# Kernel optimization log

Hardware: AMD Instinct MI355X
Metric: run time of the kernel (lower is better)

The kernel has to match this reference:

```python
import jax, jax.numpy as jnp
import numpy as np

N, M, D_IN, D_OUT = 100000, 1024, 64, 64


def setup_inputs() -> dict:
    key = jax.random.key(0)
    ks = jax.random.split(key, 8)
    # kaiming_uniform_ bound for fan_in = D_IN: sqrt(6 / fan_in) with a=sqrt(5) default? torch's
    # kaiming_uniform_ default (a=0) gives bound = sqrt(6/fan_in); exact init is irrelevant for math.
    bound = float(np.sqrt(6.0 / D_IN))
    return {
        "x": jax.random.normal(ks[0], (N, D_IN), dtype=jnp.float32),
        "neighbors": jax.random.normal(ks[1], (M, D_IN), dtype=jnp.float32),
        "Wq": jax.random.uniform(ks[2], (D_OUT, D_IN), jnp.float32, -bound, bound),
        "bq": jnp.zeros((D_OUT,), jnp.float32),
        "Wk": jax.random.uniform(ks[3], (D_OUT, D_IN), jnp.float32, -bound, bound),
        "bk": jnp.zeros((D_OUT,), jnp.float32),
        "Wv": jax.random.uniform(ks[4], (D_OUT, D_IN), jnp.float32, -bound, bound),
        "bv": jnp.zeros((D_OUT,), jnp.float32),
    }


def reference(x, neighbors, Wq, bq, Wk, bk, Wv, bv):
    # q: [N, D_OUT], k: [M, D_OUT]
    q = x @ Wq.T + bq
    k = neighbors @ Wk.T + bk
    # scores: [N, M] -- same math as sum(q[:,None,:] * k[None,:,:], axis=2) but via GEMM
    scores = q @ k.T
    attn = jax.nn.softmax(scores, axis=1)
    # attn @ neighbors: [N, D_IN], then value projection -> [N, D_OUT]
    agg = attn @ neighbors
    return agg @ Wv.T + bv
```

## Files before the change

### kernel.cpp

```cpp
#include <hip/hip_runtime.h>


#define N_ROWS 100000
#define VT_STRIDE 1040

typedef __attribute__((ext_vector_type(8))) _Float16 half8;
typedef __attribute__((ext_vector_type(4))) float    f32x4;

#define MFMA16(a,b,c) __builtin_amdgcn_mfma_f32_16x16x32_f16((a),(b),(c),0,0,0)

static __device__ __forceinline__ f32x4 zero4() {
    f32x4 v = {0.f, 0.f, 0.f, 0.f};
    return v;
}

__global__ __launch_bounds__(256)
void prep_kernel(const float* __restrict__ nb, const float* __restrict__ Wq,
                 const float* __restrict__ bq, const float* __restrict__ Wk,
                 unsigned short* __restrict__ Gh, unsigned short* __restrict__ Gl,
                 float* __restrict__ uW, unsigned short* __restrict__ Kp,
                 unsigned short* __restrict__ VTp)
{
    __shared__ __align__(16) float sm[8192];
    const int tid = threadIdx.x;
    if (blockIdx.x == 0) {
        const float4* wk4 = (const float4*)Wk;
        const float4* wq4 = (const float4*)Wq;
        float4* dk = (float4*)sm;
        float4* dq = (float4*)(sm + 4096);
        #pragma unroll
        for (int u = 0; u < 4; u++) {
            dk[u * 256 + tid] = wk4[u * 256 + tid];
            dq[u * 256 + tid] = wq4[u * 256 + tid];
        }
        __syncthreads();
        const int e2 = tid & 63, e1g = (tid >> 6) * 16;
        float g[16];
        #pragma unroll
        for (int q = 0; q < 16; q++) g[q] = 0.f;
        for (int w = 0; w < 64; w++) {
            float kv = sm[w * 64 + e2];
            const float* wqp = sm + 4096 + w * 64 + e1g;
            #pragma unroll
            for (int q = 0; q < 16; q++) g[q] = fmaf(wqp[q], kv, g[q]);
        }
        union { half8 h; uint4 u; } ph0, pl0, ph1, pl1;
        #pragma unroll
        for (int i = 0; i < 8; i++) {
            _Float16 h0 = (_Float16)g[i];
            ph0.h[i] = h0; pl0.h[i] = (_Float16)(g[i] - (float)h0);
            _Float16 h1 = (_Float16)g[8 + i];
            ph1.h[i] = h1; pl1.h[i] = (_Float16)(g[8 + i] - (float)h1);
        }
        *(uint4*)(Gh + e2 * 72 + e1g)     = ph0.u;
        *(uint4*)(Gh + e2 * 72 + e1g + 8) = ph1.u;
        *(uint4*)(Gl + e2 * 72 + e1g)     = pl0.u;
        *(uint4*)(Gl + e2 * 72 + e1g + 8) = pl1.u;
        if (tid < 64) {
            float uu = 0.f;
            for (int w = 0; w < 64; w++) uu = fmaf(bq[w], sm[w * 64 + tid], uu);
            uW[tid] = uu;
        }
    } else {
        const int j0 = (blockIdx.x - 1) * 64;
        const int jr = tid >> 2;
        const int c0 = (tid & 3) * 16;
        const float* np = nb + (size_t)(j0 + jr) * 64 + c0;
        float a[16];
        #pragma unroll
        for (int u = 0; u < 4; u++) *(float4*)(a + 4 * u) = *(const float4*)(np + 4 * u);
        const int pr = (jr & ~31) | (((jr >> 2) & 1) << 4) | (((jr >> 3) & 3) << 2) | (jr & 3);
        union { half8 h; uint4 u; } pk0, pk1;
        #pragma unroll
        for (int i = 0; i < 8; i++) { pk0.h[i] = (_Float16)a[i]; pk1.h[i] = (_Float16)a[8 + i]; }
        *(uint4*)(Kp + (size_t)(j0 + pr) * 72 + c0)     = pk0.u;
        *(uint4*)(Kp + (size_t)(j0 + pr) * 72 + c0 + 8) = pk1.u;
        #pragma unroll
        for (int i = 0; i < 16; i++) sm[jr * 65 + c0 + i] = a[i];
        __syncthreads();
        const int d   = tid >> 2;
        const int jc0 = (tid & 3) * 16;
        union { half8 h; uint4 u; } pv0, pv1;
        #pragma unroll
        for (int i = 0; i < 8; i++) {
            pv0.h[i] = (_Float16)sm[(jc0 + i) * 65 + d];
            pv1.h[i] = (_Float16)sm[(jc0 + 8 + i) * 65 + d];
        }
        *(uint4*)(VTp + (size_t)d * VT_STRIDE + j0 + jc0)     = pv0.u;
        *(uint4*)(VTp + (size_t)d * VT_STRIDE + j0 + jc0 + 8) = pv1.u;
    }
}

__global__ __launch_bounds__(256, 3)
void attn_kernel(const float* __restrict__ x,
                 const unsigned short* __restrict__ Gh,
                 const unsigned short* __restrict__ Gl,
                 const float* __restrict__ uW,
                 const unsigned short* __restrict__ Kp,
                 const unsigned short* __restrict__ VTp,
                 const float* __restrict__ Wv,
                 const float* __restrict__ bv,
                 float* __restrict__ out)
{
    __shared__ __align__(16) float slices[4 * 1088];
    const int tid  = threadIdx.x;
    const int lane = tid & 63;
    const int wv   = tid >> 6;
    const int Q    = lane >> 4;
    const int c    = lane & 15;
    const int rbase = blockIdx.x * 128 + wv * 32;
    float* slice = slices + wv * 1088;

    half8 qh[2][2], ql[2][2];
    #pragma unroll
    for (int rt = 0; rt < 2; rt++) {
        int row = rbase + rt * 16 + c;
        if (row > N_ROWS - 1) row = N_ROWS - 1;
        half8 xh[2], xl[2];
        #pragma unroll
        for (int ks = 0; ks < 2; ks++) {
            const float* xp = x + (size_t)row * 64 + ks * 32 + Q * 8;
            float a[8];
            *(float4*)a       = *(const float4*)xp;
            *(float4*)(a + 4) = *(const float4*)(xp + 4);
            #pragma unroll
            for (int i = 0; i < 8; i++) {
                _Float16 h = (_Float16)a[i];
                xh[ks][i] = h;
                xl[ks][i] = (_Float16)(a[i] - (float)h);
            }
        }
        #pragma unroll
        for (int mt = 0; mt < 4; mt++) {
            f32x4 Cm = zero4();
            #pragma unroll
            for (int ks = 0; ks < 2; ks++) {
                half8 gh = *(const half8*)(Gh + (mt * 16 + c) * 72 + ks * 32 + Q * 8);
                half8 gl = *(const half8*)(Gl + (mt * 16 + c) * 72 + ks * 32 + Q * 8);
                Cm = MFMA16(gh, xh[ks], Cm);
                Cm = MFMA16(gh, xl[ks], Cm);
                Cm = MFMA16(gl, xh[ks], Cm);
            }
            *(f32x4*)(slice + c * 68 + mt * 16 + 4 * Q) = Cm;
        }
        __builtin_amdgcn_s_waitcnt(0);
        #pragma unroll
        for (int ks = 0; ks < 2; ks++) {
            const float* qp = slice + c * 68 + ks * 32 + Q * 8;
            const float* up = uW + ks * 32 + Q * 8;
            #pragma unroll
            for (int i = 0; i < 8; i++) {
                float val = qp[i] + up[i];
                _Float16 h = (_Float16)val;
                qh[rt][ks][i] = h;
                ql[rt][ks][i] = (_Float16)(val - (float)h);
            }
        }
        __builtin_amdgcn_s_waitcnt(0);
    }

    f32x4 acc[2][4];
    #pragma unroll
    for (int qt = 0; qt < 2; qt++)
        #pragma unroll
        for (int dt = 0; dt < 4; dt++) acc[qt][dt] = zero4();
    float mrow[2] = { -3.0e38f, -3.0e38f };
    float lrow[2] = { 0.f, 0.f };

    #pragma unroll 2
    for (int jc = 0; jc < 32; jc++) {
        const int jb = jc * 32;
        half8 k0[2], k1[2];
        #pragma unroll
        for (int t = 0; t < 2; t++) {
            const unsigned short* kp = Kp + (size_t)(jb + 16 * t + c) * 72;
            k0[t] = *(const half8*)(kp + Q * 8);
            k1[t] = *(const half8*)(kp + 32 + Q * 8);
        }
        half8 vA[4];
        #pragma unroll
        for (int dt = 0; dt < 4; dt++)
            vA[dt] = *(const half8*)(VTp + (size_t)(dt * 16 + c) * VT_STRIDE + jb + Q * 8);

        f32x4 S[2][2];
        #pragma unroll
        for (int t = 0; t < 2; t++) {
            #pragma unroll
            for (int qt = 0; qt < 2; qt++) {
                f32x4 s = MFMA16(k0[t], qh[qt][0], zero4());
                s = MFMA16(k1[t], qh[qt][1], s);
                s = MFMA16(k0[t], ql[qt][0], s);
                s = MFMA16(k1[t], ql[qt][1], s);
                S[t][qt] = s;
            }
        }
        half8 pB[2];
        #pragma unroll
        for (int qt = 0; qt < 2; qt++) {
            float cm = fmaxf(fmaxf(fmaxf(S[0][qt][0], S[0][qt][1]),
                                   fmaxf(S[0][qt][2], S[0][qt][3])),
                             fmaxf(fmaxf(S[1][qt][0], S[1][qt][1]),
                                   fmaxf(S[1][qt][2], S[1][qt][3])));
            cm = fmaxf(cm, __shfl_xor(cm, 16));
            cm = fmaxf(cm, __shfl_xor(cm, 32));
            if (__any(cm > mrow[qt] + 8.f)) {
                const float mn = fmaxf(mrow[qt], cm);
                const float sc = __expf(mrow[qt] - mn);
                mrow[qt] = mn;
                lrow[qt] *= sc;
                #pragma unroll
                for (int dt = 0; dt < 4; dt++)
                    #pragma unroll
                    for (int r = 0; r < 4; r++) acc[qt][dt][r] *= sc;
            }
            const float mref = mrow[qt];
            float p[8]; float ps = 0.f;
            #pragma unroll
            for (int r = 0; r < 4; r++) { p[r] = __expf(S[0][qt][r] - mref); ps += p[r]; }
            #pragma unroll
            for (int r = 0; r < 4; r++) { p[4 + r] = __expf(S[1][qt][r] - mref); ps += p[4 + r]; }
            ps += __shfl_xor(ps, 16);
            ps += __shfl_xor(ps, 32);
            lrow[qt] += ps;
            #pragma unroll
            for (int i = 0; i < 8; i++) pB[qt][i] = (_Float16)p[i];
        }
        #pragma unroll
        for (int dt = 0; dt < 4; dt++) {
            acc[0][dt] = MFMA16(vA[dt], pB[0], acc[0][dt]);
            acc[1][dt] = MFMA16(vA[dt], pB[1], acc[1][dt]);
        }
    }

    #pragma unroll
    for (int qt = 0; qt < 2; qt++) {
        const float rl = 1.f / lrow[qt];
        #pragma unroll
        for (int dt = 0; dt < 4; dt++)
            #pragma unroll
            for (int r = 0; r < 4; r++) acc[qt][dt][r] *= rl;
    }
    half8 wf[4][2];
    #pragma unroll
    for (int mt = 0; mt < 4; mt++)
        #pragma unroll
        for (int ks = 0; ks < 2; ks++) {
            const float* wp = Wv + (size_t)(mt * 16 + c) * 64 + ks * 32 + Q * 8;
            #pragma unroll
            for (int i = 0; i < 8; i++) wf[mt][ks][i] = (_Float16)wp[i];
        }
    const int srcA = 32 * (Q & 1) + c;
    const int srcB = srcA + 16;
    const bool hi = (Q >> 1) & 1;
    f32x4 o[2][4];
    #pragma unroll
    for (int qt = 0; qt < 2; qt++) {
        half8 pe[2];
        #pragma unroll
        for (int ks = 0; ks < 2; ks++) {
            #pragma unroll
            for (int r = 0; r < 4; r++) {
                float a0 = __shfl(acc[qt][2 * ks + 0][r], srcA);
                float a1 = __shfl(acc[qt][2 * ks + 1][r], srcA);
                float b0 = __shfl(acc[qt][2 * ks + 0][r], srcB);
                float b1 = __shfl(acc[qt][2 * ks + 1][r], srcB);
                pe[ks][r]     = (_Float16)(hi ? a1 : a0);
                pe[ks][4 + r] = (_Float16)(hi ? b1 : b0);
            }
        }
        #pragma unroll
        for (int mt = 0; mt < 4; mt++) {
            f32x4 t = MFMA16(wf[mt][0], pe[0], zero4());
            o[qt][mt] = MFMA16(wf[mt][1], pe[1], t);
        }
    }
    float4 bf[4];
    #pragma unroll
    for (int mt = 0; mt < 4; mt++) bf[mt] = *(const float4*)(bv + mt * 16 + 4 * Q);
    #pragma unroll
    for (int qt = 0; qt < 2; qt++) {
        const int row = rbase + qt * 16 + c;
        if (row < N_ROWS) {
            #pragma unroll
            for (int mt = 0; mt < 4; mt++) {
                float4 vv = make_float4(o[qt][mt][0] + bf[mt].x, o[qt][mt][1] + bf[mt].y,
                                        o[qt][mt][2] + bf[mt].z, o[qt][mt][3] + bf[mt].w);
                *(float4*)(out + (size_t)row * 64 + mt * 16 + 4 * Q) = vv;
            }
        }
    }
}

extern "C" void kernel_launch(void* const* d_in, const int* in_sizes, int n_in,
                              void* d_out, int out_size, void* d_ws, size_t ws_size,
                              hipStream_t stream)
{
    const float* x  = (const float*)d_in[0];
    const float* nb = (const float*)d_in[1];
    const float* Wq = (const float*)d_in[2];
    const float* bq = (const float*)d_in[3];
    const float* Wk = (const float*)d_in[4];
    const float* Wv = (const float*)d_in[6];
    const float* bv = (const float*)d_in[7];
    float* out = (float*)d_out;

    char* ws = (char*)d_ws;
    unsigned short* Gh  = (unsigned short*)(ws);
    unsigned short* Gl  = (unsigned short*)(ws + 9216);
    float*          uW  = (float*)(ws + 18432);
    unsigned short* Kp  = (unsigned short*)(ws + 18688);
    unsigned short* VTp = (unsigned short*)(ws + 166144);

    prep_kernel<<<17, 256, 0, stream>>>(nb, Wq, bq, Wk, Gh, Gl, uW, Kp, VTp);
    const int grid = (N_ROWS + 127) / 128;
    attn_kernel<<<grid, 256, 0, stream>>>(x, Gh, Gl, uW, Kp, VTp, Wv, bv, out);
}
```

Baseline: 167.4 us.

## Use single-wave blocks, double-buffer K fragments, and defer row-sum reduction

Reshapes the attention kernel from 256-thread blocks covering 128 rows to 64-thread single-wave blocks covering 32 rows. The main loop becomes a manually double-buffered flash step that prefetches the next K tile while computing on the current one. The row-sum shuffle reduction moves out of the loop to the end, and the max shuffle now runs only when a rescale is needed. The goals are to hide K load latency and cut cross-lane shuffles per iteration, at the cost of more blocks, more register pressure from the prefetch buffers, and a grid that assumes N is divisible by 32.

```diff
diff --git a/kernel.cpp b/kernel.cpp
--- a/kernel.cpp
+++ b/kernel.cpp
@@ -91,7 +91,73 @@
     }
 }
 
-__global__ __launch_bounds__(256, 3)
+static __device__ __forceinline__ void flash_step(
+    int jb, int jn, int c, int Q,
+    const unsigned short* __restrict__ Kp, const unsigned short* __restrict__ VTp,
+    const half8 (&ck0)[2], const half8 (&ck1)[2],
+    half8 (&nk0)[2], half8 (&nk1)[2],
+    const half8 (&qh)[2][2], const half8 (&ql)[2][2],
+    f32x4 (&acc)[2][4], float (&mrow)[2], float (&lrow)[2])
+{
+    half8 vA[4];
+    #pragma unroll
+    for (int dt = 0; dt < 4; dt++)
+        vA[dt] = *(const half8*)(VTp + (size_t)(dt * 16 + c) * VT_STRIDE + jb + Q * 8);
+    #pragma unroll
+    for (int t = 0; t < 2; t++) {
+        const unsigned short* kp = Kp + (size_t)(jn + 16 * t + c) * 72;
+        nk0[t] = *(const half8*)(kp + Q * 8);
+        nk1[t] = *(const half8*)(kp + 32 + Q * 8);
+    }
+    f32x4 S[2][2];
+    #pragma unroll
+    for (int t = 0; t < 2; t++)
+        #pragma unroll
+        for (int qt = 0; qt < 2; qt++) {
+            f32x4 s = MFMA16(ck0[t], qh[qt][0], zero4());
+            s = MFMA16(ck1[t], qh[qt][1], s);
+            s = MFMA16(ck0[t], ql[qt][0], s);
+            s = MFMA16(ck1[t], ql[qt][1], s);
+            S[t][qt] = s;
+        }
+    half8 pB[2];
+    #pragma unroll
+    for (int qt = 0; qt < 2; qt++) {
+        float pmax = fmaxf(fmaxf(fmaxf(S[0][qt][0], S[0][qt][1]),
+                                 fmaxf(S[0][qt][2], S[0][qt][3])),
+                           fmaxf(fmaxf(S[1][qt][0], S[1][qt][1]),
+                                 fmaxf(S[1][qt][2], S[1][qt][3])));
+        if (__any(pmax > mrow[qt] + 8.f)) {
+            float cm = pmax;
+            cm = fmaxf(cm, __shfl_xor(cm, 16));
+            cm = fmaxf(cm, __shfl_xor(cm, 32));
+            const float mn = fmaxf(mrow[qt], cm);
+            const float sc = __expf(mrow[qt] - mn);
+            mrow[qt] = mn;
+            lrow[qt] *= sc;
+            #pragma unroll
+            for (int dt = 0; dt < 4; dt++)
+                #pragma unroll
+                for (int r = 0; r < 4; r++) acc[qt][dt][r] *= sc;
+        }
+        const float mref = mrow[qt];
+        float p[8]; float ps = 0.f;
+        #pragma unroll
+        for (int r = 0; r < 4; r++) { p[r] = __expf(S[0][qt][r] - mref); ps += p[r]; }
+        #pragma unroll
+        for (int r = 0; r < 4; r++) { p[4 + r] = __expf(S[1][qt][r] - mref); ps += p[4 + r]; }
+        lrow[qt] += ps;
+        #pragma unroll
+        for (int i = 0; i < 8; i++) pB[qt][i] = (_Float16)p[i];
+    }
+    #pragma unroll
+    for (int dt = 0; dt < 4; dt++) {
+        acc[0][dt] = MFMA16(vA[dt], pB[0], acc[0][dt]);
+        acc[1][dt] = MFMA16(vA[dt], pB[1], acc[1][dt]);
+    }
+}
+
+__global__ __launch_bounds__(64, 3)
 void attn_kernel(const float* __restrict__ x,
                  const unsigned short* __restrict__ Gh,
                  const unsigned short* __restrict__ Gl,
@@ -102,14 +168,11 @@
                  const float* __restrict__ bv,
                  float* __restrict__ out)
 {
-    __shared__ __align__(16) float slices[4 * 1088];
-    const int tid  = threadIdx.x;
-    const int lane = tid & 63;
-    const int wv   = tid >> 6;
+    __shared__ __align__(16) float slice[1088];
+    const int lane = threadIdx.x & 63;
     const int Q    = lane >> 4;
     const int c    = lane & 15;
-    const int rbase = blockIdx.x * 128 + wv * 32;
-    float* slice = slices + wv * 1088;
+    const int rbase = blockIdx.x * 32;
 
     half8 qh[2][2], ql[2][2];
     #pragma unroll
@@ -167,74 +230,27 @@
     float mrow[2] = { -3.0e38f, -3.0e38f };
     float lrow[2] = { 0.f, 0.f };
 
-    #pragma unroll 2
-    for (int jc = 0; jc < 32; jc++) {
-        const int jb = jc * 32;
-        half8 k0[2], k1[2];
-        #pragma unroll
-        for (int t = 0; t < 2; t++) {
-            const unsigned short* kp = Kp + (size_t)(jb + 16 * t + c) * 72;
-            k0[t] = *(const half8*)(kp + Q * 8);
-            k1[t] = *(const half8*)(kp + 32 + Q * 8);
-        }
-        half8 vA[4];
-        #pragma unroll
-        for (int dt = 0; dt < 4; dt++)
-            vA[dt] = *(const half8*)(VTp + (size_t)(dt * 16 + c) * VT_STRIDE + jb + Q * 8);
-
-        f32x4 S[2][2];
-        #pragma unroll
-        for (int t = 0; t < 2; t++) {
-            #pragma unroll
-            for (int qt = 0; qt < 2; qt++) {
-                f32x4 s = MFMA16(k0[t], qh[qt][0], zero4());
-                s = MFMA16(k1[t], qh[qt][1], s);
-                s = MFMA16(k0[t], ql[qt][0], s);
-                s = MFMA16(k1[t], ql[qt][1], s);
-                S[t][qt] = s;
-            }
-        }
-        half8 pB[2];
-        #pragma unroll
-        for (int qt = 0; qt < 2; qt++) {
-            float cm = fmaxf(fmaxf(fmaxf(S[0][qt][0], S[0][qt][1]),
-                                   fmaxf(S[0][qt][2], S[0][qt][3])),
-                             fmaxf(fmaxf(S[1][qt][0], S[1][qt][1]),
-                                   fmaxf(S[1][qt][2], S[1][qt][3])));
-            cm = fmaxf(cm, __shfl_xor(cm, 16));
-            cm = fmaxf(cm, __shfl_xor(cm, 32));
-            if (__any(cm > mrow[qt] + 8.f)) {
-                const float mn = fmaxf(mrow[qt], cm);
-                const float sc = __expf(mrow[qt] - mn);
-                mrow[qt] = mn;
-                lrow[qt] *= sc;
-                #pragma unroll
-                for (int dt = 0; dt < 4; dt++)
-                    #pragma unroll
-                    for (int r = 0; r < 4; r++) acc[qt][dt][r] *= sc;
-            }
-            const float mref = mrow[qt];
-            float p[8]; float ps = 0.f;
-            #pragma unroll
-            for (int r = 0; r < 4; r++) { p[r] = __expf(S[0][qt][r] - mref); ps += p[r]; }
-            #pragma unroll
-            for (int r = 0; r < 4; r++) { p[4 + r] = __expf(S[1][qt][r] - mref); ps += p[4 + r]; }
-            ps += __shfl_xor(ps, 16);
-            ps += __shfl_xor(ps, 32);
-            lrow[qt] += ps;
-            #pragma unroll
-            for (int i = 0; i < 8; i++) pB[qt][i] = (_Float16)p[i];
-        }
-        #pragma unroll
-        for (int dt = 0; dt < 4; dt++) {
-            acc[0][dt] = MFMA16(vA[dt], pB[0], acc[0][dt]);
-            acc[1][dt] = MFMA16(vA[dt], pB[1], acc[1][dt]);
-        }
+    half8 ka0[2], ka1[2], kb0[2], kb1[2];
+    #pragma unroll
+    for (int t = 0; t < 2; t++) {
+        const unsigned short* kp = Kp + (size_t)(16 * t + c) * 72;
+        ka0[t] = *(const half8*)(kp + Q * 8);
+        ka1[t] = *(const half8*)(kp + 32 + Q * 8);
+    }
+    #pragma unroll 1
+    for (int jj = 0; jj < 16; jj++) {
+        const int jb = jj * 64;
+        flash_step(jb,      jb + 32, c, Q, Kp, VTp, ka0, ka1, kb0, kb1, qh, ql, acc, mrow, lrow);
+        const int jn2 = (jb + 64 < 1024) ? jb + 64 : jb + 32;
+        flash_step(jb + 32, jn2,     c, Q, Kp, VTp, kb0, kb1, ka0, ka1, qh, ql, acc, mrow, lrow);
     }
 
     #pragma unroll
     for (int qt = 0; qt < 2; qt++) {
-        const float rl = 1.f / lrow[qt];
+        float l = lrow[qt];
+        l += __shfl_xor(l, 16);
+        l += __shfl_xor(l, 32);
+        const float rl = 1.f / l;
         #pragma unroll
         for (int dt = 0; dt < 4; dt++)
             #pragma unroll
@@ -312,6 +328,6 @@
     unsigned short* VTp = (unsigned short*)(ws + 166144);
 
     prep_kernel<<<17, 256, 0, stream>>>(nb, Wq, bq, Wk, Gh, Gl, uW, Kp, VTp);
-    const int grid = (N_ROWS + 127) / 128;
-    attn_kernel<<<grid, 256, 0, stream>>>(x, Gh, Gl, uW, Kp, VTp, Wv, bv, out);
-}
+    const int grid = N_ROWS / 32;
+    attn_kernel<<<grid, 64, 0, stream>>>(x, Gh, Gl, uW, Kp, VTp, Wv, bv, out);
+}
```

Result: faster. 161.7 us (-3.4%).
